# Performance work log

Measured on AMD Instinct MI355X. Metric: run time of the kernel, lower is better.

## Reference

```python
import jax, jax.numpy as jnp
import numpy as np

B, C, H, W = 16, 256, 128, 128
NF = 8
GN_GROUPS = 8
EPS = 1e-5


def setup_inputs() -> dict:
    key = jax.random.key(0)
    k0, k1, k2, k3 = jax.random.split(key, 4)
    return {
        "x": jax.random.normal(k0, (B, C, H, W), dtype=jnp.float32),
        # learned params
        "filter_bank": jax.random.normal(k1, (NF, 1, 7, 7), dtype=jnp.float32) * 0.02,
        "sel_w": jax.random.normal(k2, (NF, C), dtype=jnp.float32) / np.float32(np.sqrt(C)),
        "sel_b": jnp.zeros((NF,), dtype=jnp.float32),
        "proj_w": jax.random.normal(k3, (C, C, 1, 1), dtype=jnp.float32) / np.float32(np.sqrt(C)),
        "proj_b": jnp.zeros((C,), dtype=jnp.float32),
        "gn_gamma": jnp.ones((C,), dtype=jnp.float32),
        "gn_beta": jnp.zeros((C,), dtype=jnp.float32),
    }


def reference(x, filter_bank, sel_w, sel_b, proj_w, proj_b, gn_gamma, gn_beta):
    b, c, h, w = x.shape
    # filter selector: GAP -> Linear -> softmax
    pooled = x.mean(axis=(2, 3))                       # [B, C]
    weights = jax.nn.softmax(pooled @ sel_w.T + sel_b, axis=-1)  # [B, NF]
    # softmax-weighted mix of the 7x7 filter bank -> one filter per sample
    combined = jnp.einsum('bn,nhw->bhw', weights, filter_bank[:, 0])  # [B, 7, 7]
    # per-sample depthwise conv: each sample's filter applied to all C channels
    kern = jnp.repeat(combined[:, None], c, axis=0)    # [B*C, 1, 7, 7] (sample-major, matches reshape)
    filtered = jax.lax.conv_general_dilated(
        x.reshape(1, b * c, h, w), kern,
        window_strides=(1, 1), padding=((3, 3), (3, 3)),
        feature_group_count=b * c,
        dimension_numbers=('NCHW', 'OIHW', 'NCHW'),
    ).reshape(b, c, h, w)
    # output projection: 1x1 conv
    y = jnp.einsum('bchw,oc->bohw', filtered, proj_w[:, :, 0, 0]) + proj_b[None, :, None, None]
    # GroupNorm(8, C) with affine
    yg = y.reshape(b, GN_GROUPS, c // GN_GROUPS, h, w)
    mean = yg.mean(axis=(2, 3, 4), keepdims=True)
    var = yg.var(axis=(2, 3, 4), keepdims=True)
    yn = ((yg - mean) * jax.lax.rsqrt(var + EPS)).reshape(b, c, h, w)
    yn = yn * gn_gamma[None, :, None, None] + gn_beta[None, :, None, None]
    # exact GELU (torch default) + residual
    return jax.nn.gelu(yn, approximate=False) + x
```

## Files before the change

kernel.cpp:

```cpp
#include <hip/hip_runtime.h>
#include <math.h>

#define BB 16
#define CC 256
#define HH 128
#define WW 128
#define HWSZ 16384
#define NF 8
#define EPSV 1e-5f

typedef __attribute__((ext_vector_type(8))) short short8;
typedef __attribute__((ext_vector_type(4))) float f32x4;

static __device__ __forceinline__ unsigned short f2bf(float f) {
  unsigned int u = __float_as_uint(f);
  u += 0x7fffu + ((u >> 16) & 1u);
  return (unsigned short)(u >> 16);
}

static __device__ __forceinline__ float bf2f(unsigned int h) {
  return __uint_as_float(h << 16);
}

static __device__ __forceinline__ void gload_lds16(const unsigned short* g,
                                                   unsigned short* l) {
  __builtin_amdgcn_global_load_lds(
      (const __attribute__((address_space(1))) void*)(size_t)g,
      (__attribute__((address_space(3))) void*)(unsigned)(size_t)l, 16, 0, 0);
}

__global__ __launch_bounds__(256) void pool_pack_kernel(
    const float* __restrict__ x, const float* __restrict__ pw,
    float* __restrict__ pooled, unsigned short* __restrict__ ap) {
  int blk = blockIdx.x;
  int tid = threadIdx.x;
  if (blk >= BB * CC) {
    int idx = (blk - BB * CC) * 256 + tid;
    int e = idx & 7;
    int lane = (idx >> 3) & 63;
    int kb = (idx >> 9) & 7;
    int mb = idx >> 12;
    int o = mb * 16 + (lane & 15);
    int c = kb * 32 + (lane >> 4) * 8 + e;
    ap[idx] = f2bf(pw[o * 256 + c]);
    return;
  }
  const float4* xp = (const float4*)(x + (size_t)blk * HWSZ);
  float s = 0.f;
#pragma unroll
  for (int i = 0; i < 16; ++i) {
    float4 v = xp[tid + i * 256];
    s += v.x + v.y + v.z + v.w;
  }
#pragma unroll
  for (int off = 32; off > 0; off >>= 1) s += __shfl_down(s, off, 64);
  __shared__ float ls[4];
  if ((tid & 63) == 0) ls[tid >> 6] = s;
  __syncthreads();
  if (tid == 0) pooled[blk] = (ls[0] + ls[1] + ls[2] + ls[3]) * (1.0f / 16384.0f);
}

__global__ __launch_bounds__(256) void selector_kernel(
    const float* __restrict__ pooled, const float* __restrict__ sel_w,
    const float* __restrict__ sel_b, const float* __restrict__ fbank,
    float* __restrict__ combined) {
  int tid = threadIdx.x;
  __shared__ float lg[BB][NF];
  __shared__ float wsm[BB][NF];
  if (tid < BB * NF) {
    int b = tid >> 3, n = tid & 7;
    const float* p = pooled + b * CC;
    const float* w = sel_w + n * CC;
    float d = sel_b[n];
    for (int c = 0; c < CC; c += 4) {
      d += p[c] * w[c] + p[c + 1] * w[c + 1] + p[c + 2] * w[c + 2] + p[c + 3] * w[c + 3];
    }
    lg[b][n] = d;
  }
  __syncthreads();
  if (tid < BB) {
    int b = tid;
    float m = lg[b][0];
#pragma unroll
    for (int n = 1; n < NF; ++n) m = fmaxf(m, lg[b][n]);
    float e[NF];
    float s = 0.f;
#pragma unroll
    for (int n = 0; n < NF; ++n) { e[n] = expf(lg[b][n] - m); s += e[n]; }
    float inv = 1.0f / s;
#pragma unroll
    for (int n = 0; n < NF; ++n) wsm[b][n] = e[n] * inv;
  }
  __syncthreads();
  for (int i = tid; i < BB * 49; i += 256) {
    int b = i / 49, j = i % 49;
    float acc = 0.f;
#pragma unroll
    for (int n = 0; n < NF; ++n) acc += wsm[b][n] * fbank[n * 49 + j];
    combined[b * 64 + j] = acc;
  }
}

#define TR 32
__global__ __launch_bounds__(256) void dwconv_kernel(
    const float* __restrict__ x, const float* __restrict__ combined,
    unsigned short* __restrict__ fbp) {
  int plane = blockIdx.x;
  int rt = blockIdx.y;
  int b = plane >> 8;
  int r0 = rt * TR;
  int tid = threadIdx.x;

  __shared__ float xs[TR + 6][136];

  float kf[49];
  {
    const float* cb = combined + b * 64;
#pragma unroll
    for (int i = 0; i < 49; ++i) kf[i] = cb[i];
  }

  const size_t pbase = (size_t)plane * HWSZ;
  for (int idx = tid; idx < (TR + 6) * 34; idx += 256) {
    int row = idx / 34;
    int seg = idx % 34;
    int r = r0 - 3 + row;
    int c = seg * 4 - 4;
    float4 v = make_float4(0.f, 0.f, 0.f, 0.f);
    if (r >= 0 && r < HH && c >= 0 && c < WW) {
      v = *(const float4*)(x + pbase + (size_t)r * WW + c);
    }
    *(float4*)&xs[row][seg * 4] = v;
  }
  __syncthreads();

  int cg = tid & 31;
  int rg = tid >> 5;
  float acc[4][4] = {};

#pragma unroll
  for (int ri = 0; ri < 10; ++ri) {
    int lrow = 4 * rg + ri;
    float xr[12];
#pragma unroll
    for (int s = 0; s < 3; ++s)
      *(float4*)&xr[4 * s] = *(const float4*)&xs[lrow][cg * 4 + 4 * s];
#pragma unroll
    for (int orr = 0; orr < 4; ++orr) {
      int dy = ri - orr;
      if (dy < 0 || dy > 6) continue;
#pragma unroll
      for (int oc = 0; oc < 4; ++oc) {
#pragma unroll
        for (int dx = 0; dx < 7; ++dx) {
          acc[orr][oc] += xr[oc + dx + 1] * kf[dy * 7 + dx];
        }
      }
    }
  }

#pragma unroll
  for (int orr = 0; orr < 4; ++orr) {
    ushort4 sv;
    sv.x = f2bf(acc[orr][0]);
    sv.y = f2bf(acc[orr][1]);
    sv.z = f2bf(acc[orr][2]);
    sv.w = f2bf(acc[orr][3]);
    *(ushort4*)(fbp + pbase + (size_t)(r0 + 4 * rg + orr) * WW + 4 * cg) = sv;
  }
}

__global__ __launch_bounds__(256) void transpose_kernel(
    const unsigned short* __restrict__ fb, unsigned short* __restrict__ fbT) {
  int bid = blockIdx.x;
  int bs = bid >> 10;
  int cs = (bid >> 8) & 3;
  int ps = bid & 255;
  int t = threadIdx.x;

  __shared__ unsigned int Ts[64][33];

  int cpair = t >> 3;
  int pch = t & 7;
  const unsigned short* s =
      fb + ((size_t)bs * CC + cs * 64 + 2 * cpair) * HWSZ + ps * 64 + pch * 8;
  uint4 A0 = *(const uint4*)s;
  uint4 A1 = *(const uint4*)(s + HWSZ);
  unsigned int wa[4] = {A0.x, A0.y, A0.z, A0.w};
  unsigned int wb[4] = {A1.x, A1.y, A1.z, A1.w};
#pragma unroll
  for (int i = 0; i < 8; ++i) {
    int p = pch * 8 + i;
    unsigned int lo = (wa[i >> 1] >> ((i & 1) * 16)) & 0xffffu;
    unsigned int hi = (wb[i >> 1] >> ((i & 1) * 16)) & 0xffffu;
    Ts[p][cpair] = lo | (hi << 16);
  }
  __syncthreads();

  size_t obase = ((size_t)bs * HWSZ + (size_t)ps * 64) * 256 + cs * 64;
#pragma unroll
  for (int r = 0; r < 2; ++r) {
    int chunk = t + 256 * r;
    int p = chunk >> 3, ch = chunk & 7;
    uint4 v;
    v.x = Ts[p][ch * 4];
    v.y = Ts[p][ch * 4 + 1];
    v.z = Ts[p][ch * 4 + 2];
    v.w = Ts[p][ch * 4 + 3];
    *(uint4*)(fbT + obase + (size_t)p * 256 + ch * 8) = v;
  }
}

#define SWZ(p) ((((p) >> 1) ^ ((p) >> 4)) & 3)

__global__ __launch_bounds__(512, 2) void gemm_kernel(
    const unsigned short* __restrict__ fbT, const unsigned short* __restrict__ ap,
    const float* __restrict__ proj_b, unsigned short* __restrict__ yb,
    float* __restrict__ part) {
  int bid = blockIdx.x;
  int bs = bid >> 7;
  int pt = bid & 127;
  int p0 = pt * 128;
  int tid = threadIdx.x;
  int lane = tid & 63;
  int wave = tid >> 6;
  int wm = wave >> 1;
  int wn = wave & 1;

  __shared__ __align__(16) unsigned short A_lds[2][8192];
  __shared__ __align__(16) unsigned short B_lds[2][4096];

  const unsigned short* asrc0 =
      ap + (size_t)(tid >> 6) * 4096 + (size_t)(tid & 63) * 8;
  unsigned short* adst = &A_lds[0][0] + (size_t)tid * 8;
  int sp = tid >> 2;
  int sj = (tid & 3) ^ SWZ(sp);
  const unsigned short* bsrc0 =
      fbT + ((size_t)bs * HWSZ + p0 + sp) * 256 + sj * 8;
  unsigned short* bdst = &B_lds[0][0] + (size_t)tid * 8;

#define STAGE(kb, buf)                                                        \
  do {                                                                        \
    gload_lds16(asrc0 + (size_t)(kb) * 512, adst + (size_t)(buf) * 8192);     \
    gload_lds16(asrc0 + 32768 + (size_t)(kb) * 512,                           \
                adst + (size_t)(buf) * 8192 + 4096);                          \
    gload_lds16(bsrc0 + (size_t)(kb) * 32, bdst + (size_t)(buf) * 4096);      \
  } while (0)

  STAGE(0, 0);
  STAGE(1, 1);

  f32x4 acc[4][4];
#pragma unroll
  for (int mb = 0; mb < 4; ++mb)
#pragma unroll
    for (int nb = 0; nb < 4; ++nb) acc[mb][nb] = (f32x4){0.f, 0.f, 0.f, 0.f};

  int aofs[4];
#pragma unroll
  for (int mb = 0; mb < 4; ++mb) aofs[mb] = ((wm * 4 + mb) * 64 + lane) * 8;
  int bofs[4];
#pragma unroll
  for (int nb = 0; nb < 4; ++nb) {
    int pp = wn * 64 + nb * 16 + (lane & 15);
    bofs[nb] = pp * 32 + (((lane >> 4) * 8) ^ (SWZ(pp) << 3));
  }

#pragma unroll
  for (int kb = 0; kb < 8; ++kb) {
    const int cur = kb & 1;
    if (kb < 7) {
      asm volatile("s_waitcnt vmcnt(3)" ::: "memory");
    } else {
      asm volatile("s_waitcnt vmcnt(0)" ::: "memory");
    }
    __builtin_amdgcn_s_barrier();

    short8 af[4], bfr[4];
#pragma unroll
    for (int mb = 0; mb < 4; ++mb)
      af[mb] = *(const short8*)(&A_lds[cur][0] + aofs[mb]);
#pragma unroll
    for (int nb = 0; nb < 4; ++nb)
      bfr[nb] = *(const short8*)(&B_lds[cur][0] + bofs[nb]);
    asm volatile("s_waitcnt lgkmcnt(0)" ::: "memory");
    __builtin_amdgcn_sched_barrier(0);
    __builtin_amdgcn_s_barrier();

    if (kb < 6) STAGE(kb + 2, cur);
    __builtin_amdgcn_sched_barrier(0);

#pragma unroll
    for (int mb = 0; mb < 4; ++mb)
#pragma unroll
      for (int nb = 0; nb < 4; ++nb)
        acc[mb][nb] = __builtin_amdgcn_mfma_f32_16x16x32_bf16(
            af[mb], bfr[nb], acc[mb][nb], 0, 0, 0);
  }

  float psum[2] = {0.f, 0.f}, psq[2] = {0.f, 0.f};
  int orl = (lane >> 4) * 4;
  int pl = lane & 15;
  const size_t ybase = (size_t)bs * CC * HWSZ + p0 + wn * 64;
  int obase = wm * 64;
#pragma unroll
  for (int mb = 0; mb < 4; ++mb) {
    int gi = mb >> 1;
#pragma unroll
    for (int r = 0; r < 4; ++r) {
      int o = obase + mb * 16 + orl + r;
      float pb = proj_b[o];
      unsigned short* yrow = yb + ybase + (size_t)o * HWSZ + pl;
#pragma unroll
      for (int nb = 0; nb < 4; ++nb) {
        float v = acc[mb][nb][r] + pb;
        yrow[nb * 16] = f2bf(v);
        psum[gi] += v;
        psq[gi] += v * v;
      }
    }
  }
#pragma unroll
  for (int off = 32; off > 0; off >>= 1) {
#pragma unroll
    for (int k = 0; k < 2; ++k) {
      psum[k] += __shfl_down(psum[k], off, 64);
      psq[k] += __shfl_down(psq[k], off, 64);
    }
  }
  if (lane == 0) {
#pragma unroll
    for (int k = 0; k < 2; ++k) {
      int bg = bs * 8 + wm * 2 + k;
      part[(size_t)bg * 256 + pt * 2 + wn] = psum[k];
      part[32768 + (size_t)bg * 256 + pt * 2 + wn] = psq[k];
    }
  }
#undef STAGE
}

__global__ __launch_bounds__(256) void reduce_kernel(
    const float* __restrict__ part, float* __restrict__ stats) {
  int bg = blockIdx.x;
  int t = threadIdx.x;
  float s = part[(size_t)bg * 256 + t];
  float q = part[32768 + (size_t)bg * 256 + t];
#pragma unroll
  for (int off = 32; off > 0; off >>= 1) {
    s += __shfl_down(s, off, 64);
    q += __shfl_down(q, off, 64);
  }
  __shared__ float ls[8];
  if ((t & 63) == 0) { ls[t >> 6] = s; ls[4 + (t >> 6)] = q; }
  __syncthreads();
  if (t == 0) stats[bg] = ls[0] + ls[1] + ls[2] + ls[3];
  if (t == 64) stats[128 + bg] = ls[4] + ls[5] + ls[6] + ls[7];
}

__global__ __launch_bounds__(256) void out_kernel(
    const float* __restrict__ x, const unsigned short* __restrict__ yb,
    const float* __restrict__ stats, const float* __restrict__ gamma,
    const float* __restrict__ beta, float* __restrict__ out) {
  int plane = blockIdx.x;
  int b = plane >> 8, c = plane & 255, g = c >> 5;
  const float inv_n = 1.0f / (32.0f * (float)HWSZ);
  float mean = stats[b * 8 + g] * inv_n;
  float var = stats[128 + b * 8 + g] * inv_n - mean * mean;
  float rstd = rsqrtf(var + EPSV);
  float scale = gamma[c] * rstd;
  float shift = beta[c] - mean * scale;

  const size_t base = (size_t)plane * HWSZ;
  for (int i = threadIdx.x; i < HWSZ / 8; i += 256) {
    uint4 yv = *(const uint4*)(yb + base + 8 * (size_t)i);
    float4 x0 = *(const float4*)(x + base + 8 * (size_t)i);
    float4 x1 = *(const float4*)(x + base + 8 * (size_t)i + 4);
    unsigned int yw[4] = {yv.x, yv.y, yv.z, yv.w};
    float r[8];
    float xr[8] = {x0.x, x0.y, x0.z, x0.w, x1.x, x1.y, x1.z, x1.w};
#pragma unroll
    for (int k = 0; k < 8; ++k) {
      unsigned int h = (yw[k >> 1] >> ((k & 1) * 16)) & 0xffffu;
      float t = bf2f(h) * scale + shift;
      float ge = 0.5f * t * (1.0f + erff(t * 0.70710678118654752f));
      r[k] = ge + xr[k];
    }
    *(float4*)(out + base + 8 * (size_t)i) = make_float4(r[0], r[1], r[2], r[3]);
    *(float4*)(out + base + 8 * (size_t)i + 4) = make_float4(r[4], r[5], r[6], r[7]);
  }
}

extern "C" void kernel_launch(void* const* d_in, const int* in_sizes, int n_in,
                              void* d_out, int out_size, void* d_ws, size_t ws_size,
                              hipStream_t stream) {
  const float* x      = (const float*)d_in[0];
  const float* fbank  = (const float*)d_in[1];
  const float* sel_w  = (const float*)d_in[2];
  const float* sel_b  = (const float*)d_in[3];
  const float* proj_w = (const float*)d_in[4];
  const float* proj_b = (const float*)d_in[5];
  const float* gamma  = (const float*)d_in[6];
  const float* beta   = (const float*)d_in[7];
  float* out = (float*)d_out;

  unsigned short* fb  = (unsigned short*)d_ws;
  unsigned short* yb  = fb;
  unsigned short* fbT = fb + (size_t)BB * CC * HWSZ;
  unsigned short* apk = fbT + (size_t)BB * CC * HWSZ;
  float* pooled   = (float*)(apk + 65536);
  float* combined = pooled + BB * CC;
  float* stats    = combined + BB * 64;
  float* part     = stats + 256;

  hipLaunchKernelGGL(pool_pack_kernel, dim3(BB * CC + 256), dim3(256), 0, stream,
                     x, proj_w, pooled, apk);
  hipLaunchKernelGGL(selector_kernel, dim3(1), dim3(256), 0, stream,
                     pooled, sel_w, sel_b, fbank, combined);
  hipLaunchKernelGGL(dwconv_kernel, dim3(BB * CC, HH / TR), dim3(256), 0, stream,
                     x, combined, fb);
  hipLaunchKernelGGL(transpose_kernel, dim3(BB * 4 * 256), dim3(256), 0, stream,
                     fb, fbT);
  hipLaunchKernelGGL(gemm_kernel, dim3(BB * 128), dim3(512), 0, stream,
                     fbT, apk, proj_b, yb, part);
  hipLaunchKernelGGL(reduce_kernel, dim3(128), dim3(256), 0, stream, part, stats);
  hipLaunchKernelGGL(out_kernel, dim3(BB * CC), dim3(256), 0, stream,
                     x, yb, stats, gamma, beta, out);
}
```

Before: 454.6 us.

## Fuse channel-to-pixel transpose into GEMM B-tile staging via register loads

Removes the separate transpose kernel and instead has the GEMM load the channel-major bf16 filtered tensor directly into registers, then repack channel pairs into the swizzled pixel-major LDS layout for the B operand. This avoids a full extra write and read of a 128 MiB intermediate plus one kernel launch. In exchange, B staging no longer uses direct global-to-LDS loads, so it adds register traffic, scalar LDS stores and an extra barrier per k-step. The global reads are also narrower (8-byte per thread, strided by channel), which may lower GEMM efficiency. The workspace layout changes so yb no longer aliases fb.

```diff
diff --git a/kernel.cpp b/kernel.cpp
--- a/kernel.cpp
+++ b/kernel.cpp
@@ -170,51 +170,10 @@
   }
 }
 
-__global__ __launch_bounds__(256) void transpose_kernel(
-    const unsigned short* __restrict__ fb, unsigned short* __restrict__ fbT) {
-  int bid = blockIdx.x;
-  int bs = bid >> 10;
-  int cs = (bid >> 8) & 3;
-  int ps = bid & 255;
-  int t = threadIdx.x;
-
-  __shared__ unsigned int Ts[64][33];
-
-  int cpair = t >> 3;
-  int pch = t & 7;
-  const unsigned short* s =
-      fb + ((size_t)bs * CC + cs * 64 + 2 * cpair) * HWSZ + ps * 64 + pch * 8;
-  uint4 A0 = *(const uint4*)s;
-  uint4 A1 = *(const uint4*)(s + HWSZ);
-  unsigned int wa[4] = {A0.x, A0.y, A0.z, A0.w};
-  unsigned int wb[4] = {A1.x, A1.y, A1.z, A1.w};
-#pragma unroll
-  for (int i = 0; i < 8; ++i) {
-    int p = pch * 8 + i;
-    unsigned int lo = (wa[i >> 1] >> ((i & 1) * 16)) & 0xffffu;
-    unsigned int hi = (wb[i >> 1] >> ((i & 1) * 16)) & 0xffffu;
-    Ts[p][cpair] = lo | (hi << 16);
-  }
-  __syncthreads();
-
-  size_t obase = ((size_t)bs * HWSZ + (size_t)ps * 64) * 256 + cs * 64;
-#pragma unroll
-  for (int r = 0; r < 2; ++r) {
-    int chunk = t + 256 * r;
-    int p = chunk >> 3, ch = chunk & 7;
-    uint4 v;
-    v.x = Ts[p][ch * 4];
-    v.y = Ts[p][ch * 4 + 1];
-    v.z = Ts[p][ch * 4 + 2];
-    v.w = Ts[p][ch * 4 + 3];
-    *(uint4*)(fbT + obase + (size_t)p * 256 + ch * 8) = v;
-  }
-}
-
 #define SWZ(p) ((((p) >> 1) ^ ((p) >> 4)) & 3)
 
 __global__ __launch_bounds__(512, 2) void gemm_kernel(
-    const unsigned short* __restrict__ fbT, const unsigned short* __restrict__ ap,
+    const unsigned short* __restrict__ fb, const unsigned short* __restrict__ ap,
     const float* __restrict__ proj_b, unsigned short* __restrict__ yb,
     float* __restrict__ part) {
   int bid = blockIdx.x;
@@ -233,22 +192,44 @@
   const unsigned short* asrc0 =
       ap + (size_t)(tid >> 6) * 4096 + (size_t)(tid & 63) * 8;
   unsigned short* adst = &A_lds[0][0] + (size_t)tid * 8;
-  int sp = tid >> 2;
-  int sj = (tid & 3) ^ SWZ(sp);
+
+  int cp = tid >> 5;
+  int pq = tid & 31;
   const unsigned short* bsrc0 =
-      fbT + ((size_t)bs * HWSZ + p0 + sp) * 256 + sj * 8;
-  unsigned short* bdst = &B_lds[0][0] + (size_t)tid * 8;
-
-#define STAGE(kb, buf)                                                        \
+      fb + ((size_t)bs * CC + 2 * cp) * HWSZ + p0 + 4 * pq;
+
+  uint2 bregs[2][2];
+
+#define STAGE_A(kb, buf)                                                      \
   do {                                                                        \
     gload_lds16(asrc0 + (size_t)(kb) * 512, adst + (size_t)(buf) * 8192);     \
     gload_lds16(asrc0 + 32768 + (size_t)(kb) * 512,                           \
                 adst + (size_t)(buf) * 8192 + 4096);                          \
-    gload_lds16(bsrc0 + (size_t)(kb) * 32, bdst + (size_t)(buf) * 4096);      \
   } while (0)
-
-  STAGE(0, 0);
-  STAGE(1, 1);
+#define LOAD_B(kb, slot)                                                      \
+  do {                                                                        \
+    const unsigned short* s_ = bsrc0 + (size_t)(kb) * 32 * HWSZ;              \
+    bregs[slot][0] = *(const uint2*)s_;                                       \
+    bregs[slot][1] = *(const uint2*)(s_ + HWSZ);                              \
+  } while (0)
+#define WRITE_B(slot, buf)                                                    \
+  do {                                                                        \
+    unsigned int w0_[2] = {bregs[slot][0].x, bregs[slot][0].y};               \
+    unsigned int w1_[2] = {bregs[slot][1].x, bregs[slot][1].y};               \
+    _Pragma("unroll")                                                         \
+    for (int j_ = 0; j_ < 4; ++j_) {                                          \
+      int p_ = 4 * pq + j_;                                                   \
+      int cc_ = (2 * cp) ^ (SWZ(p_) << 3);                                    \
+      unsigned int lo_ = (w0_[j_ >> 1] >> ((j_ & 1) * 16)) & 0xffffu;         \
+      unsigned int hi_ = (w1_[j_ >> 1] >> ((j_ & 1) * 16)) & 0xffffu;         \
+      *(unsigned int*)&B_lds[buf][p_ * 32 + cc_] = lo_ | (hi_ << 16);         \
+    }                                                                         \
+  } while (0)
+
+  STAGE_A(0, 0);
+  LOAD_B(0, 0);
+  STAGE_A(1, 1);
+  LOAD_B(1, 1);
 
   f32x4 acc[4][4];
 #pragma unroll
@@ -266,16 +247,14 @@
     bofs[nb] = pp * 32 + (((lane >> 4) * 8) ^ (SWZ(pp) << 3));
   }
 
+  asm volatile("s_waitcnt vmcnt(4)" ::: "memory");
+  WRITE_B(0, 0);
+  asm volatile("s_waitcnt lgkmcnt(0)" ::: "memory");
+  __builtin_amdgcn_s_barrier();
+
 #pragma unroll
   for (int kb = 0; kb < 8; ++kb) {
     const int cur = kb & 1;
-    if (kb < 7) {
-      asm volatile("s_waitcnt vmcnt(3)" ::: "memory");
-    } else {
-      asm volatile("s_waitcnt vmcnt(0)" ::: "memory");
-    }
-    __builtin_amdgcn_s_barrier();
-
     short8 af[4], bfr[4];
 #pragma unroll
     for (int mb = 0; mb < 4; ++mb)
@@ -287,8 +266,21 @@
     __builtin_amdgcn_sched_barrier(0);
     __builtin_amdgcn_s_barrier();
 
-    if (kb < 6) STAGE(kb + 2, cur);
-    __builtin_amdgcn_sched_barrier(0);
+    if (kb < 6) {
+      STAGE_A(kb + 2, cur);
+      LOAD_B(kb + 2, cur);
+      __builtin_amdgcn_sched_barrier(0);
+    }
+    if (kb < 6) {
+      asm volatile("s_waitcnt vmcnt(4)" ::: "memory");
+    } else if (kb == 6) {
+      asm volatile("s_waitcnt vmcnt(0)" ::: "memory");
+    }
+    if (kb < 7) {
+      WRITE_B(cur ^ 1, cur ^ 1);
+      asm volatile("s_waitcnt lgkmcnt(0)" ::: "memory");
+      __builtin_amdgcn_s_barrier();
+    }
 
 #pragma unroll
     for (int mb = 0; mb < 4; ++mb)
@@ -336,7 +328,9 @@
       part[32768 + (size_t)bg * 256 + pt * 2 + wn] = psq[k];
     }
   }
-#undef STAGE
+#undef STAGE_A
+#undef LOAD_B
+#undef WRITE_B
 }
 
 __global__ __launch_bounds__(256) void reduce_kernel(
@@ -404,9 +398,8 @@
   float* out = (float*)d_out;
 
   unsigned short* fb  = (unsigned short*)d_ws;
-  unsigned short* yb  = fb;
-  unsigned short* fbT = fb + (size_t)BB * CC * HWSZ;
-  unsigned short* apk = fbT + (size_t)BB * CC * HWSZ;
+  unsigned short* yb  = fb + (size_t)BB * CC * HWSZ;
+  unsigned short* apk = yb + (size_t)BB * CC * HWSZ;
   float* pooled   = (float*)(apk + 65536);
   float* combined = pooled + BB * CC;
   float* stats    = combined + BB * 64;
@@ -418,10 +411,8 @@
                      pooled, sel_w, sel_b, fbank, combined);
   hipLaunchKernelGGL(dwconv_kernel, dim3(BB * CC, HH / TR), dim3(256), 0, stream,
                      x, combined, fb);
-  hipLaunchKernelGGL(transpose_kernel, dim3(BB * 4 * 256), dim3(256), 0, stream,
-                     fb, fbT);
   hipLaunchKernelGGL(gemm_kernel, dim3(BB * 128), dim3(512), 0, stream,
-                     fbT, apk, proj_b, yb, part);
+                     fb, apk, proj_b, yb, part);
   hipLaunchKernelGGL(reduce_kernel, dim3(128), dim3(256), 0, stream, part, stats);
   hipLaunchKernelGGL(out_kernel, dim3(BB * CC), dim3(256), 0, stream,
                      x, yb, stats, gamma, beta, out);
```

Measured after the change: 428.0 us. 5.9% less time.
